# Performance work log

Measured on AMD Instinct MI355X. Metric: run time of the kernel, lower is better.

The kernel has to match this reference:

```python
import jax, jax.numpy as jnp
import numpy as np

NUM_TOKENS = 8192
EMBED_DIM = 32
BETA = 1.0
DECAY = 0.99
L2_EPS = 1e-12  # torch F.normalize denom clamp


def l2norm(t):
    return t / jnp.maximum(jnp.linalg.norm(t, axis=-1, keepdims=True), L2_EPS)


def setup_inputs() -> dict:
    key = jax.random.key(0)
    k1, k2 = jax.random.split(key)
    z = jax.random.normal(k1, (32, EMBED_DIM, 16, 16), dtype=jnp.float32)  # [B, C, H, W]
    embedding = l2norm(jax.random.normal(k2, (NUM_TOKENS, EMBED_DIM), dtype=jnp.float32))
    cluster_sizes = jnp.zeros((NUM_TOKENS,), dtype=jnp.float32)
    return {"z": z, "embedding": embedding, "cluster_sizes": cluster_sizes}


def reference(z, embedding, cluster_sizes):
    B, C, H, W = z.shape
    zc = jnp.transpose(z, (0, 2, 3, 1))          # channel_last: [B, H, W, C]
    zn = l2norm(zc)
    z_flat = zn.reshape(-1, C)                   # [N, C], N = B*H*W

    # nearest centroid by cosine similarity (codebook rows are unit norm)
    cos_sim = z_flat @ embedding.T               # [N, K]
    token_ids = jnp.argmax(cos_sim, axis=-1)     # [N]
    z_q_flat = embedding[token_ids]              # gather, [N, C]
    z_q = z_q_flat.reshape(zn.shape)

    # EMA statistics (training branch; one-hot @ matmuls expressed as scatter-adds)
    bins = jnp.zeros((NUM_TOKENS,), z.dtype).at[token_ids].add(1.0)      # encodings.sum(0)
    new_cluster_sizes = cluster_sizes * DECAY + (1.0 - DECAY) * bins
    zero_mask = bins == 0
    bins_c = jnp.where(zero_mask, 1.0, bins)
    embed_sum = jnp.zeros((NUM_TOKENS, C), z.dtype).at[token_ids].add(z_flat)  # (z_flat.T @ onehot).T
    embed_normalized = l2norm(embed_sum / bins_c[:, None])
    embed_normalized = jnp.where(zero_mask[:, None], embedding, embed_normalized)
    new_embedding = l2norm(embedding * DECAY + (1.0 - DECAY) * embed_normalized)

    # commitment loss + straight-through estimator
    loss = BETA * jnp.mean((jax.lax.stop_gradient(z_q) - zn) ** 2)
    z_q_st = zn + jax.lax.stop_gradient(z_q - zn)
    z_q_out = jnp.transpose(z_q_st, (0, 3, 1, 2))  # back to [B, C, H, W]

    return (z_q_out, loss, token_ids.reshape(B, H, W), new_embedding, new_cluster_sizes)
```

## Files before the change

### kernel.cpp

```cpp
#include <hip/hip_runtime.h>


#define NTOK   8192
#define NCODE  8192
#define CDIM   32
#define HW     256
#define DECAYF 0.99f
#define EPSF   0.01f

#define OUT_ZQ   0
#define OUT_LOSS 262144
#define OUT_IDS  262145
#define OUT_EMB  270337
#define OUT_CS   532481

#define WS_ZN     0u
#define WS_ZNT    1048576u
#define WS_PMAX   2097152u
#define WS_PACK   3145728u
#define WS_BINS   3211264u
#define WS_LOSS   3244032u
#define WS_ZEND   3244036u
#define WS_ZERO_BYTES (WS_ZEND - WS_PACK)
#define WS_IDS    3244036u
#define WS_POS    3276804u
#define WS_OFFS   3309572u
#define WS_SORTED 3342340u

#define CHUNK  256
#define NCHUNK (NCODE / CHUNK)
#define TILES  (CHUNK / 16)

typedef __attribute__((ext_vector_type(8))) short bf16x8;
typedef __attribute__((ext_vector_type(4))) float f32x4;

__device__ inline unsigned short f2bf(float x) {
    unsigned u = __float_as_uint(x);
    return (unsigned short)((u + 0x7FFFu + ((u >> 16) & 1u)) >> 16);
}
__device__ inline unsigned fmap(float s) {
    unsigned u = __float_as_uint(s);
    return (u & 0x80000000u) ? ~u : (u | 0x80000000u);
}

__global__ __launch_bounds__(256) void k_prep(const float* __restrict__ z,
                                              float* __restrict__ zn,
                                              float* __restrict__ znT) {
    int n = blockIdx.x * 256 + threadIdx.x;
    int b = n >> 8, hw = n & 255;
    const float* zp = z + (size_t)b * (CDIM * HW) + hw;
    float v[CDIM];
    float ss = 0.f;
#pragma unroll
    for (int c = 0; c < CDIM; ++c) {
        float t = zp[c * HW];
        v[c] = t;
        ss += t * t;
    }
    float d = fmaxf(sqrtf(ss), 1e-12f);
    float* o = zn + (size_t)n * CDIM;
#pragma unroll
    for (int c = 0; c < CDIM; ++c) {
        float t = v[c] / d;
        o[c] = t;
        znT[(size_t)c * NTOK + n] = t;
    }
}

__device__ inline void stage_emb_bf16(const float* __restrict__ emb, int kbase,
                                      unsigned short* lbs) {
    const float4* src = (const float4*)(emb + (size_t)kbase * CDIM);
    ushort4* dst = (ushort4*)lbs;
#pragma unroll
    for (int i = 0; i < 8; ++i) {
        int j = threadIdx.x + i * 256;
        float4 v = src[j];
        ushort4 h;
        h.x = f2bf(v.x); h.y = f2bf(v.y); h.z = f2bf(v.z); h.w = f2bf(v.w);
        dst[j] = h;
    }
}

__device__ inline void load_afrags(const float* __restrict__ zn, int wtok,
                                   int col, int quad, bf16x8* a) {
#pragma unroll
    for (int f = 0; f < 4; ++f) {
        const float4* zp =
            (const float4*)(zn + (size_t)(wtok + f * 16 + col) * CDIM + quad * 8);
        float4 x = zp[0], y = zp[1];
        bf16x8 v;
        v[0] = (short)f2bf(x.x); v[1] = (short)f2bf(x.y);
        v[2] = (short)f2bf(x.z); v[3] = (short)f2bf(x.w);
        v[4] = (short)f2bf(y.x); v[5] = (short)f2bf(y.y);
        v[6] = (short)f2bf(y.z); v[7] = (short)f2bf(y.w);
        a[f] = v;
    }
}

__global__ __launch_bounds__(256) void k_max(const float* __restrict__ zn,
                                             const float* __restrict__ emb,
                                             float* __restrict__ pmax) {
    __shared__ unsigned short lbs[CHUNK * CDIM];
    __shared__ float lmax[256];
    int kbase = blockIdx.y * CHUNK;
    stage_emb_bf16(emb, kbase, lbs);
    __syncthreads();

    int wave = threadIdx.x >> 6, lane = threadIdx.x & 63;
    int col = lane & 15, quad = lane >> 4;
    int wtok = blockIdx.x * 256 + wave * 64;

    bf16x8 a[4];
    load_afrags(zn, wtok, col, quad, a);

    const bf16x8* bl = (const bf16x8*)lbs;
    const f32x4 zero4 = {0.f, 0.f, 0.f, 0.f};
    float m[4][4];
#pragma unroll
    for (int f = 0; f < 4; ++f)
#pragma unroll
        for (int r = 0; r < 4; ++r) m[f][r] = -1e30f;

    for (int t = 0; t < TILES; ++t) {
        bf16x8 b = bl[(t * 16 + col) * 4 + quad];
#pragma unroll
        for (int f = 0; f < 4; ++f) {
            f32x4 d = __builtin_amdgcn_mfma_f32_16x16x32_bf16(a[f], b, zero4, 0, 0, 0);
#pragma unroll
            for (int r = 0; r < 4; ++r) m[f][r] = fmaxf(m[f][r], d[r]);
        }
    }
#pragma unroll
    for (int f = 0; f < 4; ++f)
#pragma unroll
        for (int r = 0; r < 4; ++r) {
            float v = m[f][r];
#pragma unroll
            for (int s = 1; s < 16; s <<= 1) v = fmaxf(v, __shfl_xor(v, s));
            if (col == 0) lmax[wave * 64 + f * 16 + quad * 4 + r] = v;
        }
    __syncthreads();
    pmax[(size_t)blockIdx.y * NTOK + blockIdx.x * 256 + threadIdx.x] =
        lmax[threadIdx.x];
}

__global__ __launch_bounds__(256) void k_pick(const float* __restrict__ zn,
                                              const float* __restrict__ emb,
                                              const float* __restrict__ pmax,
                                              unsigned long long* __restrict__ packed) {
    __shared__ unsigned short lbs[CHUNK * CDIM];
    __shared__ float lthr[256];
    int kbase = blockIdx.y * CHUNK;
    stage_emb_bf16(emb, kbase, lbs);
    {
        int tok = blockIdx.x * 256 + threadIdx.x;
        float mx = -1e30f;
#pragma unroll
        for (int ch = 0; ch < NCHUNK; ++ch)
            mx = fmaxf(mx, pmax[(size_t)ch * NTOK + tok]);
        lthr[threadIdx.x] = mx - EPSF;
    }
    __syncthreads();

    int wave = threadIdx.x >> 6, lane = threadIdx.x & 63;
    int col = lane & 15, quad = lane >> 4;
    int wtok = blockIdx.x * 256 + wave * 64;

    bf16x8 a[4];
    load_afrags(zn, wtok, col, quad, a);

    float thr[4][4];
#pragma unroll
    for (int f = 0; f < 4; ++f)
#pragma unroll
        for (int r = 0; r < 4; ++r)
            thr[f][r] = lthr[wave * 64 + f * 16 + quad * 4 + r];

    const bf16x8* bl = (const bf16x8*)lbs;
    const f32x4 zero4 = {0.f, 0.f, 0.f, 0.f};

    for (int t = 0; t < TILES; ++t) {
        bf16x8 b = bl[(t * 16 + col) * 4 + quad];
#pragma unroll
        for (int f = 0; f < 4; ++f) {
            f32x4 d = __builtin_amdgcn_mfma_f32_16x16x32_bf16(a[f], b, zero4, 0, 0, 0);
#pragma unroll
            for (int r = 0; r < 4; ++r) {
                if (d[r] >= thr[f][r]) {
                    int tok = wtok + f * 16 + quad * 4 + r;
                    int code = kbase + t * 16 + col;
                    const float* zp = zn + (size_t)tok * CDIM;
                    const float* ep = emb + (size_t)code * CDIM;
                    float a0 = 0.f, a1 = 0.f, a2 = 0.f, a3 = 0.f;
#pragma unroll
                    for (int j = 0; j < 8; ++j) {
                        a0 = __builtin_fmaf(zp[4 * j + 0], ep[4 * j + 0], a0);
                        a1 = __builtin_fmaf(zp[4 * j + 1], ep[4 * j + 1], a1);
                        a2 = __builtin_fmaf(zp[4 * j + 2], ep[4 * j + 2], a2);
                        a3 = __builtin_fmaf(zp[4 * j + 3], ep[4 * j + 3], a3);
                    }
                    float s = (a0 + a1) + (a2 + a3);
                    atomicMax(packed + tok, ((unsigned long long)fmap(s) << 13) |
                                            (unsigned long long)(8191 - code));
                }
            }
        }
    }
}

__global__ __launch_bounds__(256) void k_postzq(const unsigned long long* __restrict__ packed,
                                                const float* __restrict__ znT,
                                                const float* __restrict__ emb,
                                                int* __restrict__ bins,
                                                int* __restrict__ ids,
                                                int* __restrict__ pos,
                                                float* __restrict__ out,
                                                float* __restrict__ loss_acc) {
    if (blockIdx.x >= 1024) {
        int n = (blockIdx.x - 1024) * 256 + threadIdx.x;
        int id = 8191 - (int)(packed[n] & 8191ull);
        ids[n] = id;
        out[OUT_IDS + n] = (float)id;
        pos[n] = atomicAdd(bins + id, 1);
        return;
    }
    __shared__ float lsum[4];
    int b = blockIdx.x >> 5, c = blockIdx.x & 31;
    int hw = threadIdx.x;
    int n = b * 256 + hw;
    int id = 8191 - (int)(packed[n] & 8191ull);
    float ev = emb[(size_t)id * CDIM + c];
    float zv = znT[(size_t)c * NTOK + n];
    out[OUT_ZQ + ((size_t)b * CDIM + c) * HW + hw] = ev;
    float dd = ev - zv;
    float s = dd * dd;
#pragma unroll
    for (int off = 32; off > 0; off >>= 1) s += __shfl_down(s, off);
    if ((hw & 63) == 0) lsum[hw >> 6] = s;
    __syncthreads();
    if (hw == 0)
        atomicAdd(loss_acc, lsum[0] + lsum[1] + lsum[2] + lsum[3]);
}

__global__ __launch_bounds__(1024) void k_scanplace(const int* __restrict__ bins,
                                                    const int* __restrict__ ids,
                                                    const int* __restrict__ pos,
                                                    int* __restrict__ offs,
                                                    int* __restrict__ sorted) {
    __shared__ int sc[2][1024];
    int t = threadIdx.x;
    int loc[8];
    int s = 0;
#pragma unroll
    for (int i = 0; i < 8; ++i) {
        loc[i] = s;
        s += bins[t * 8 + i];
    }
    sc[0][t] = s;
    __syncthreads();
    int src = 0;
    for (int d = 1; d < 1024; d <<= 1) {
        sc[1 - src][t] = sc[src][t] + (t >= d ? sc[src][t - d] : 0);
        src ^= 1;
        __syncthreads();
    }
    int excl = sc[src][t] - s;
#pragma unroll
    for (int i = 0; i < 8; ++i) offs[t * 8 + i] = excl + loc[i];
    __syncthreads();
    for (int n = t; n < NTOK; n += 1024)
        sorted[offs[ids[n]] + pos[n]] = n;
}

__global__ __launch_bounds__(256) void k_update(const float* __restrict__ zn,
                                                const float* __restrict__ emb,
                                                const float* __restrict__ cs,
                                                const int* __restrict__ bins,
                                                const int* __restrict__ offs,
                                                const int* __restrict__ sorted,
                                                const float* __restrict__ loss_acc,
                                                float* __restrict__ out) {
    int idx = blockIdx.x * 256 + threadIdx.x;
    int k = idx >> 5, c = idx & 31;
    int bi = bins[k];
    int off = offs[k];
    float t = 0.f;
    for (int i = 0; i < bi; ++i) {
        int n = sorted[off + i];
        t += zn[(size_t)n * CDIM + c];
    }
    float bf = (float)bi;
    bool zero = (bi == 0);
    t /= (zero ? 1.0f : bf);
    float ss = t * t;
#pragma unroll
    for (int s = 1; s < 32; s <<= 1) ss += __shfl_xor(ss, s);
    float d = fmaxf(sqrtf(ss), 1e-12f);
    float ew = emb[idx];
    float en = zero ? ew : (t / d);
    float w = ew * DECAYF + (1.0f - DECAYF) * en;
    float ss2 = w * w;
#pragma unroll
    for (int s = 1; s < 32; s <<= 1) ss2 += __shfl_xor(ss2, s);
    float d2 = fmaxf(sqrtf(ss2), 1e-12f);
    out[OUT_EMB + idx] = w / d2;
    if (c == 0) out[OUT_CS + k] = cs[k] * DECAYF + (1.0f - DECAYF) * bf;
    if (idx == 0) out[OUT_LOSS] = loss_acc[0] * (1.0f / 262144.0f);
}

extern "C" void kernel_launch(void* const* d_in, const int* in_sizes, int n_in,
                              void* d_out, int out_size, void* d_ws, size_t ws_size,
                              hipStream_t stream) {
    const float* z   = (const float*)d_in[0];
    const float* emb = (const float*)d_in[1];
    const float* cs  = (const float*)d_in[2];
    float* out = (float*)d_out;
    char* ws = (char*)d_ws;

    float* zn                  = (float*)(ws + WS_ZN);
    float* znT                 = (float*)(ws + WS_ZNT);
    float* pmax                = (float*)(ws + WS_PMAX);
    unsigned long long* packed = (unsigned long long*)(ws + WS_PACK);
    int* bins                  = (int*)(ws + WS_BINS);
    float* loss_acc            = (float*)(ws + WS_LOSS);
    int* ids                   = (int*)(ws + WS_IDS);
    int* pos                   = (int*)(ws + WS_POS);
    int* offs                  = (int*)(ws + WS_OFFS);
    int* sorted                = (int*)(ws + WS_SORTED);

    hipMemsetAsync(ws + WS_PACK, 0, WS_ZERO_BYTES, stream);

    k_prep<<<dim3(NTOK / 256), 256, 0, stream>>>(z, zn, znT);
    k_max<<<dim3(NTOK / 256, NCHUNK), 256, 0, stream>>>(zn, emb, pmax);
    k_pick<<<dim3(NTOK / 256, NCHUNK), 256, 0, stream>>>(zn, emb, pmax, packed);
    k_postzq<<<dim3(1056), 256, 0, stream>>>(packed, znT, emb, bins, ids, pos, out, loss_acc);
    k_scanplace<<<dim3(1), 1024, 0, stream>>>(bins, ids, pos, offs, sorted);
    k_update<<<dim3(1024), 256, 0, stream>>>(zn, emb, cs, bins, offs, sorted, loss_acc, out);
}
```

Baseline: 146.4 us.

## Replace second MFMA pass with candidate-chunk list and exact fp32 rescoring

The old version ran the full bf16 MFMA similarity pass twice: once for per-chunk maxima and again to find near-max candidates. Now a gather kernel builds a compact list of (token, chunk) pairs whose chunk max lies within the epsilon of the global max. A rescoring kernel then computes exact fp32 dot products only for those chunks, using a block-wide reduction and a single atomicMax. The prep kernel also pre-converts the normalized inputs and the codebook to bf16 once, and loss accumulation is spread across 64 partial slots to reduce atomic contention. In exchange, rescoring cost depends on how many candidate chunks survive, and there is an extra launch plus a global atomic counter.

After: 163.7 us. 1.12x slower.

```diff
diff --git a/kernel.cpp b/kernel.cpp
--- a/kernel.cpp
+++ b/kernel.cpp
@@ -15,17 +15,20 @@
 #define OUT_CS   532481
 
 #define WS_ZN     0u
-#define WS_ZNT    1048576u
+#define WS_ZNBF   1048576u
+#define WS_EBF    1572864u
 #define WS_PMAX   2097152u
 #define WS_PACK   3145728u
 #define WS_BINS   3211264u
-#define WS_LOSS   3244032u
-#define WS_ZEND   3244036u
+#define WS_LOSSP  3244032u
+#define WS_CNT    3244288u
+#define WS_ZEND   3244292u
 #define WS_ZERO_BYTES (WS_ZEND - WS_PACK)
-#define WS_IDS    3244036u
-#define WS_POS    3276804u
-#define WS_OFFS   3309572u
-#define WS_SORTED 3342340u
+#define WS_IDS    3244292u
+#define WS_POS    3277060u
+#define WS_OFFS   3309828u
+#define WS_SORTED 3342596u
+#define WS_LIST   3375364u
 
 #define CHUNK  256
 #define NCHUNK (NCODE / CHUNK)
@@ -44,66 +47,55 @@
 }
 
 __global__ __launch_bounds__(256) void k_prep(const float* __restrict__ z,
+                                              const float* __restrict__ emb,
                                               float* __restrict__ zn,
-                                              float* __restrict__ znT) {
-    int n = blockIdx.x * 256 + threadIdx.x;
-    int b = n >> 8, hw = n & 255;
-    const float* zp = z + (size_t)b * (CDIM * HW) + hw;
-    float v[CDIM];
-    float ss = 0.f;
-#pragma unroll
-    for (int c = 0; c < CDIM; ++c) {
-        float t = zp[c * HW];
-        v[c] = t;
-        ss += t * t;
-    }
-    float d = fmaxf(sqrtf(ss), 1e-12f);
-    float* o = zn + (size_t)n * CDIM;
-#pragma unroll
-    for (int c = 0; c < CDIM; ++c) {
-        float t = v[c] / d;
-        o[c] = t;
-        znT[(size_t)c * NTOK + n] = t;
-    }
-}
-
-__device__ inline void stage_emb_bf16(const float* __restrict__ emb, int kbase,
-                                      unsigned short* lbs) {
-    const float4* src = (const float4*)(emb + (size_t)kbase * CDIM);
-    ushort4* dst = (ushort4*)lbs;
-#pragma unroll
-    for (int i = 0; i < 8; ++i) {
-        int j = threadIdx.x + i * 256;
-        float4 v = src[j];
-        ushort4 h;
-        h.x = f2bf(v.x); h.y = f2bf(v.y); h.z = f2bf(v.z); h.w = f2bf(v.w);
-        dst[j] = h;
-    }
-}
-
-__device__ inline void load_afrags(const float* __restrict__ zn, int wtok,
-                                   int col, int quad, bf16x8* a) {
-#pragma unroll
-    for (int f = 0; f < 4; ++f) {
-        const float4* zp =
-            (const float4*)(zn + (size_t)(wtok + f * 16 + col) * CDIM + quad * 8);
-        float4 x = zp[0], y = zp[1];
-        bf16x8 v;
-        v[0] = (short)f2bf(x.x); v[1] = (short)f2bf(x.y);
-        v[2] = (short)f2bf(x.z); v[3] = (short)f2bf(x.w);
-        v[4] = (short)f2bf(y.x); v[5] = (short)f2bf(y.y);
-        v[6] = (short)f2bf(y.z); v[7] = (short)f2bf(y.w);
-        a[f] = v;
-    }
-}
-
-__global__ __launch_bounds__(256) void k_max(const float* __restrict__ zn,
-                                             const float* __restrict__ emb,
+                                              unsigned short* __restrict__ znbf,
+                                              unsigned short* __restrict__ ebf) {
+    if (blockIdx.x < 32) {
+        int n = blockIdx.x * 256 + threadIdx.x;
+        int b = n >> 8, hw = n & 255;
+        const float* zp = z + (size_t)b * (CDIM * HW) + hw;
+        float v[CDIM];
+        float ss = 0.f;
+#pragma unroll
+        for (int c = 0; c < CDIM; ++c) {
+            float t = zp[c * HW];
+            v[c] = t;
+            ss += t * t;
+        }
+        float d = fmaxf(sqrtf(ss), 1e-12f);
+        float* o = zn + (size_t)n * CDIM;
+        unsigned short* ob = znbf + (size_t)n * CDIM;
+#pragma unroll
+        for (int c = 0; c < CDIM; ++c) {
+            float t = v[c] / d;
+            o[c] = t;
+            ob[c] = f2bf(t);
+        }
+    } else {
+        int base = (blockIdx.x - 32) * 2048 + threadIdx.x * 8;
+        const float4* s = (const float4*)(emb + base);
+        float4 x = s[0], y = s[1];
+        ushort4 u0 = {f2bf(x.x), f2bf(x.y), f2bf(x.z), f2bf(x.w)};
+        ushort4 u1 = {f2bf(y.x), f2bf(y.y), f2bf(y.z), f2bf(y.w)};
+        *(ushort4*)(ebf + base) = u0;
+        *(ushort4*)(ebf + base + 4) = u1;
+    }
+}
+
+__global__ __launch_bounds__(256) void k_max(const unsigned short* __restrict__ znbf,
+                                             const unsigned short* __restrict__ ebf,
                                              float* __restrict__ pmax) {
     __shared__ unsigned short lbs[CHUNK * CDIM];
     __shared__ float lmax[256];
     int kbase = blockIdx.y * CHUNK;
-    stage_emb_bf16(emb, kbase, lbs);
+    {
+        const float4* src = (const float4*)(ebf + (size_t)kbase * CDIM);
+        float4* dst = (float4*)lbs;
+#pragma unroll
+        for (int j = 0; j < 4; ++j)
+            dst[threadIdx.x + j * 256] = src[threadIdx.x + j * 256];
+    }
     __syncthreads();
 
     int wave = threadIdx.x >> 6, lane = threadIdx.x & 63;
@@ -111,7 +103,9 @@
     int wtok = blockIdx.x * 256 + wave * 64;
 
     bf16x8 a[4];
-    load_afrags(zn, wtok, col, quad, a);
+#pragma unroll
+    for (int f = 0; f < 4; ++f)
+        a[f] = *(const bf16x8*)(znbf + (size_t)(wtok + f * 16 + col) * CDIM + quad * 8);
 
     const bf16x8* bl = (const bf16x8*)lbs;
     const f32x4 zero4 = {0.f, 0.f, 0.f, 0.f};
@@ -140,82 +134,97 @@
             if (col == 0) lmax[wave * 64 + f * 16 + quad * 4 + r] = v;
         }
     __syncthreads();
-    pmax[(size_t)blockIdx.y * NTOK + blockIdx.x * 256 + threadIdx.x] =
-        lmax[threadIdx.x];
-}
-
-__global__ __launch_bounds__(256) void k_pick(const float* __restrict__ zn,
-                                              const float* __restrict__ emb,
-                                              const float* __restrict__ pmax,
-                                              unsigned long long* __restrict__ packed) {
-    __shared__ unsigned short lbs[CHUNK * CDIM];
-    __shared__ float lthr[256];
-    int kbase = blockIdx.y * CHUNK;
-    stage_emb_bf16(emb, kbase, lbs);
-    {
-        int tok = blockIdx.x * 256 + threadIdx.x;
-        float mx = -1e30f;
-#pragma unroll
-        for (int ch = 0; ch < NCHUNK; ++ch)
-            mx = fmaxf(mx, pmax[(size_t)ch * NTOK + tok]);
-        lthr[threadIdx.x] = mx - EPSF;
-    }
-    __syncthreads();
-
-    int wave = threadIdx.x >> 6, lane = threadIdx.x & 63;
-    int col = lane & 15, quad = lane >> 4;
-    int wtok = blockIdx.x * 256 + wave * 64;
-
-    bf16x8 a[4];
-    load_afrags(zn, wtok, col, quad, a);
-
-    float thr[4][4];
-#pragma unroll
-    for (int f = 0; f < 4; ++f)
-#pragma unroll
-        for (int r = 0; r < 4; ++r)
-            thr[f][r] = lthr[wave * 64 + f * 16 + quad * 4 + r];
-
-    const bf16x8* bl = (const bf16x8*)lbs;
-    const f32x4 zero4 = {0.f, 0.f, 0.f, 0.f};
-
-    for (int t = 0; t < TILES; ++t) {
-        bf16x8 b = bl[(t * 16 + col) * 4 + quad];
-#pragma unroll
-        for (int f = 0; f < 4; ++f) {
-            f32x4 d = __builtin_amdgcn_mfma_f32_16x16x32_bf16(a[f], b, zero4, 0, 0, 0);
-#pragma unroll
-            for (int r = 0; r < 4; ++r) {
-                if (d[r] >= thr[f][r]) {
-                    int tok = wtok + f * 16 + quad * 4 + r;
-                    int code = kbase + t * 16 + col;
-                    const float* zp = zn + (size_t)tok * CDIM;
-                    const float* ep = emb + (size_t)code * CDIM;
-                    float a0 = 0.f, a1 = 0.f, a2 = 0.f, a3 = 0.f;
-#pragma unroll
-                    for (int j = 0; j < 8; ++j) {
-                        a0 = __builtin_fmaf(zp[4 * j + 0], ep[4 * j + 0], a0);
-                        a1 = __builtin_fmaf(zp[4 * j + 1], ep[4 * j + 1], a1);
-                        a2 = __builtin_fmaf(zp[4 * j + 2], ep[4 * j + 2], a2);
-                        a3 = __builtin_fmaf(zp[4 * j + 3], ep[4 * j + 3], a3);
-                    }
-                    float s = (a0 + a1) + (a2 + a3);
-                    atomicMax(packed + tok, ((unsigned long long)fmap(s) << 13) |
-                                            (unsigned long long)(8191 - code));
-                }
-            }
-        }
+    pmax[(size_t)blockIdx.y * NTOK + blockIdx.x * 256 + threadIdx.x] = lmax[threadIdx.x];
+}
+
+__global__ __launch_bounds__(256) void k_gmax(const float* __restrict__ pmax,
+                                              unsigned* __restrict__ list,
+                                              unsigned* __restrict__ cnt) {
+    int tok = blockIdx.x * 256 + threadIdx.x;
+    float pm[NCHUNK];
+    float mx = -1e30f;
+#pragma unroll
+    for (int ch = 0; ch < NCHUNK; ++ch) {
+        pm[ch] = pmax[(size_t)ch * NTOK + tok];
+        mx = fmaxf(mx, pm[ch]);
+    }
+    float thr = mx - EPSF;
+    int nq = 0;
+#pragma unroll
+    for (int ch = 0; ch < NCHUNK; ++ch) nq += (pm[ch] >= thr) ? 1 : 0;
+
+    __shared__ int sc[256];
+    int t = threadIdx.x;
+    sc[t] = nq;
+    __syncthreads();
+    for (int d = 1; d < 256; d <<= 1) {
+        int v = sc[t] + ((t >= d) ? sc[t - d] : 0);
+        __syncthreads();
+        sc[t] = v;
+        __syncthreads();
+    }
+    int incl = sc[t];
+    __shared__ unsigned base;
+    if (t == 255) base = atomicAdd(cnt, (unsigned)incl);
+    __syncthreads();
+    unsigned w = base + (unsigned)(incl - nq);
+#pragma unroll
+    for (int ch = 0; ch < NCHUNK; ++ch)
+        if (pm[ch] >= thr) list[w++] = ((unsigned)tok << 5) | (unsigned)ch;
+}
+
+__global__ __launch_bounds__(256) void k_rescore(const unsigned* __restrict__ list,
+                                                 const unsigned* __restrict__ cnt,
+                                                 const float* __restrict__ zn,
+                                                 const float* __restrict__ emb,
+                                                 unsigned long long* __restrict__ packed) {
+    __shared__ unsigned long long wk[4];
+    unsigned n = cnt[0];
+    if (n > 32u * 8192u) n = 32u * 8192u;
+    int lane = threadIdx.x & 63, wid = threadIdx.x >> 6;
+    for (unsigned e = blockIdx.x; e < n; e += gridDim.x) {
+        unsigned ent = list[e];
+        unsigned tok = ent >> 5, ch = ent & 31u;
+        unsigned code = ch * 256u + threadIdx.x;
+        const float* zp = zn + (size_t)tok * CDIM;
+        const float* ep = emb + (size_t)code * CDIM;
+        float a0 = 0.f, a1 = 0.f, a2 = 0.f, a3 = 0.f;
+#pragma unroll
+        for (int j = 0; j < 8; ++j) {
+            a0 = __builtin_fmaf(zp[4 * j + 0], ep[4 * j + 0], a0);
+            a1 = __builtin_fmaf(zp[4 * j + 1], ep[4 * j + 1], a1);
+            a2 = __builtin_fmaf(zp[4 * j + 2], ep[4 * j + 2], a2);
+            a3 = __builtin_fmaf(zp[4 * j + 3], ep[4 * j + 3], a3);
+        }
+        float s = (a0 + a1) + (a2 + a3);
+        unsigned long long key = ((unsigned long long)fmap(s) << 13) |
+                                 (unsigned long long)(8191u - code);
+#pragma unroll
+        for (int sh = 1; sh < 64; sh <<= 1) {
+            unsigned long long o = __shfl_xor(key, sh);
+            key = (o > key) ? o : key;
+        }
+        if (lane == 0) wk[wid] = key;
+        __syncthreads();
+        if (threadIdx.x == 0) {
+            unsigned long long k0 = wk[0];
+            if (wk[1] > k0) k0 = wk[1];
+            if (wk[2] > k0) k0 = wk[2];
+            if (wk[3] > k0) k0 = wk[3];
+            atomicMax(packed + tok, k0);
+        }
+        __syncthreads();
     }
 }
 
 __global__ __launch_bounds__(256) void k_postzq(const unsigned long long* __restrict__ packed,
-                                                const float* __restrict__ znT,
+                                                const float* __restrict__ zn,
                                                 const float* __restrict__ emb,
                                                 int* __restrict__ bins,
                                                 int* __restrict__ ids,
                                                 int* __restrict__ pos,
                                                 float* __restrict__ out,
-                                                float* __restrict__ loss_acc) {
+                                                float* __restrict__ loss_part) {
     if (blockIdx.x >= 1024) {
         int n = (blockIdx.x - 1024) * 256 + threadIdx.x;
         int id = 8191 - (int)(packed[n] & 8191ull);
@@ -230,7 +239,7 @@
     int n = b * 256 + hw;
     int id = 8191 - (int)(packed[n] & 8191ull);
     float ev = emb[(size_t)id * CDIM + c];
-    float zv = znT[(size_t)c * NTOK + n];
+    float zv = zn[(size_t)n * CDIM + c];
     out[OUT_ZQ + ((size_t)b * CDIM + c) * HW + hw] = ev;
     float dd = ev - zv;
     float s = dd * dd;
@@ -239,7 +248,8 @@
     if ((hw & 63) == 0) lsum[hw >> 6] = s;
     __syncthreads();
     if (hw == 0)
-        atomicAdd(loss_acc, lsum[0] + lsum[1] + lsum[2] + lsum[3]);
+        atomicAdd(loss_part + (blockIdx.x & 63),
+                  lsum[0] + lsum[1] + lsum[2] + lsum[3]);
 }
 
 __global__ __launch_bounds__(1024) void k_scanplace(const int* __restrict__ bins,
@@ -278,9 +288,15 @@
                                                 const int* __restrict__ bins,
                                                 const int* __restrict__ offs,
                                                 const int* __restrict__ sorted,
-                                                const float* __restrict__ loss_acc,
+                                                const float* __restrict__ loss_part,
                                                 float* __restrict__ out) {
     int idx = blockIdx.x * 256 + threadIdx.x;
+    if (blockIdx.x == 0 && threadIdx.x < 64) {
+        float lp = loss_part[threadIdx.x];
+#pragma unroll
+        for (int sh = 32; sh > 0; sh >>= 1) lp += __shfl_down(lp, sh);
+        if (threadIdx.x == 0) out[OUT_LOSS] = lp * (1.0f / 262144.0f);
+    }
     int k = idx >> 5, c = idx & 31;
     int bi = bins[k];
     int off = offs[k];
@@ -305,7 +321,6 @@
     float d2 = fmaxf(sqrtf(ss2), 1e-12f);
     out[OUT_EMB + idx] = w / d2;
     if (c == 0) out[OUT_CS + k] = cs[k] * DECAYF + (1.0f - DECAYF) * bf;
-    if (idx == 0) out[OUT_LOSS] = loss_acc[0] * (1.0f / 262144.0f);
 }
 
 extern "C" void kernel_launch(void* const* d_in, const int* in_sizes, int n_in,
@@ -318,22 +333,26 @@
     char* ws = (char*)d_ws;
 
     float* zn                  = (float*)(ws + WS_ZN);
-    float* znT                 = (float*)(ws + WS_ZNT);
+    unsigned short* znbf       = (unsigned short*)(ws + WS_ZNBF);
+    unsigned short* ebf        = (unsigned short*)(ws + WS_EBF);
     float* pmax                = (float*)(ws + WS_PMAX);
     unsigned long long* packed = (unsigned long long*)(ws + WS_PACK);
     int* bins                  = (int*)(ws + WS_BINS);
-    float* loss_acc            = (float*)(ws + WS_LOSS);
+    float* loss_part           = (float*)(ws + WS_LOSSP);
+    unsigned* cnt              = (unsigned*)(ws + WS_CNT);
     int* ids                   = (int*)(ws + WS_IDS);
     int* pos                   = (int*)(ws + WS_POS);
     int* offs                  = (int*)(ws + WS_OFFS);
     int* sorted                = (int*)(ws + WS_SORTED);
+    unsigned* list             = (unsigned*)(ws + WS_LIST);
 
     hipMemsetAsync(ws + WS_PACK, 0, WS_ZERO_BYTES, stream);
 
-    k_prep<<<dim3(NTOK / 256), 256, 0, stream>>>(z, zn, znT);
-    k_max<<<dim3(NTOK / 256, NCHUNK), 256, 0, stream>>>(zn, emb, pmax);
-    k_pick<<<dim3(NTOK / 256, NCHUNK), 256, 0, stream>>>(zn, emb, pmax, packed);
-    k_postzq<<<dim3(1056), 256, 0, stream>>>(packed, znT, emb, bins, ids, pos, out, loss_acc);
+    k_prep<<<dim3(160), 256, 0, stream>>>(z, emb, zn, znbf, ebf);
+    k_max<<<dim3(NTOK / 256, NCHUNK), 256, 0, stream>>>(znbf, ebf, pmax);
+    k_gmax<<<dim3(NTOK / 256), 256, 0, stream>>>(pmax, list, cnt);
+    k_rescore<<<dim3(512), 256, 0, stream>>>(list, cnt, zn, emb, packed);
+    k_postzq<<<dim3(1056), 256, 0, stream>>>(packed, zn, emb, bins, ids, pos, out, loss_part);
     k_scanplace<<<dim3(1), 1024, 0, stream>>>(bins, ids, pos, offs, sorted);
-    k_update<<<dim3(1024), 256, 0, stream>>>(zn, emb, cs, bins, offs, sorted, loss_acc, out);
-}
+    k_update<<<dim3(1024), 256, 0, stream>>>(zn, emb, cs, bins, offs, sorted, loss_part, out);
+}
```
